# Kernel tuning notes

Hardware: AMD Instinct MI355X
Metric: run time of the kernel (lower is better)

Reference implementation:

```python
import jax, jax.numpy as jnp
import numpy as np

CLUSTER_TEMP = 5.0


def setup_inputs() -> dict:
    key = jax.random.key(0)
    ks = jax.random.split(key, 8)
    n, d_in, h, d, K = 50000, 512, 1024, 256, 64
    s = lambda f: 1.0 / np.sqrt(f)
    return {
        "x": jax.random.normal(ks[0], (n, d_in), dtype=jnp.float32),
        "W1": jax.random.normal(ks[1], (d_in, h), dtype=jnp.float32) * s(d_in),
        "b1": jnp.zeros((h,), jnp.float32),
        "W2": jax.random.normal(ks[2], (h, h), dtype=jnp.float32) * s(h),
        "b2": jnp.zeros((h,), jnp.float32),
        "W3": jax.random.normal(ks[3], (h, d), dtype=jnp.float32) * s(h),
        "b3": jnp.zeros((d,), jnp.float32),
        "mu_init": jax.random.normal(ks[4], (K, d), dtype=jnp.float32),
        "num_iter": 10,
    }


def reference(x, W1, b1, W2, b2, W3, b3, mu_init, num_iter):
    # MLP embed: ReLU on all but last layer
    h1 = jax.nn.relu(x @ W1 + b1)
    h2 = jax.nn.relu(h1 @ W2 + b2)
    embeds = h2 @ W3 + b3                      # [n, d]

    # row-wise L2 normalize (torch.diag(1/norm) @ data == row scaling)
    data = embeds / jnp.linalg.norm(embeds, axis=1, keepdims=True)

    def step(mu, _):
        dist = data @ mu.T                     # [n, K]
        r = jax.nn.softmax(CLUSTER_TEMP * dist, axis=1)
        cluster_r = r.sum(axis=0)              # [K]
        cluster_mean = jnp.einsum('nk,nd->kd', r, data)  # [K, d]
        new_mu = cluster_mean / cluster_r[:, None]       # diag(1/cluster_r) @ mean
        return new_mu, None

    mu, _ = jax.lax.scan(step, mu_init, None, length=num_iter)
    dist = data @ mu.T
    r = jax.nn.softmax(CLUSTER_TEMP * dist, axis=1)      # forward returns r only
    return r
```

## Files before the change

### kernel.cpp

```cpp
#include <hip/hip_runtime.h>
#include <math.h>

#define CLUSTER_TEMP 5.0f
#define NSPL 16

typedef __attribute__((ext_vector_type(8))) short bf16x8;
typedef __attribute__((ext_vector_type(4))) float f32x4;

__device__ __forceinline__ unsigned short f2bf(float f) {
  unsigned u = __float_as_uint(f);
  u += 0x7fff + ((u >> 16) & 1);
  return (unsigned short)(u >> 16);
}
__device__ __forceinline__ float bf2f(unsigned short s) {
  return __uint_as_float((unsigned)s << 16);
}

typedef const __attribute__((address_space(1))) void* gas_t;
typedef __attribute__((address_space(3))) void* las_t;
__device__ __forceinline__ void gload16(const void* g, void* l) {
  __builtin_amdgcn_global_load_lds((gas_t)g, (las_t)l, 16, 0, 0);
}

__global__ __launch_bounds__(256)
void wprep(const float* __restrict__ W, unsigned short* __restrict__ hi,
           unsigned short* __restrict__ lo, int K, int N)
{
  __shared__ float tile[32][33];
  const int bx = blockIdx.x * 32;
  const int by = blockIdx.y * 32;
  const int tx = threadIdx.x, ty = threadIdx.y;
#pragma unroll
  for (int i = 0; i < 4; ++i)
    tile[ty + i*8][tx] = W[(size_t)(by + ty + i*8)*N + bx + tx];
  __syncthreads();
#pragma unroll
  for (int i = 0; i < 4; ++i) {
    const int nn = bx + ty + i*8;
    const int kk = by + tx;
    const float v = tile[tx][ty + i*8];
    const unsigned short h = f2bf(v);
    hi[(size_t)nn*K + kk] = h;
    lo[(size_t)nn*K + kk] = f2bf(v - bf2f(h));
  }
}

template<int INMODE, bool RELU, bool PAIR_OUT>
__global__ __launch_bounds__(256, 2)
void gemm_pair(const float* __restrict__ Af,
               const unsigned short* __restrict__ Ah, const unsigned short* __restrict__ Al,
               const unsigned short* __restrict__ Bh, const unsigned short* __restrict__ Bl,
               const float* __restrict__ bias,
               unsigned short* __restrict__ Ch, unsigned short* __restrict__ Cl,
               float* __restrict__ Cf,
               int M, int N, int K)
{
  __shared__ unsigned short As_h[128][32];
  __shared__ unsigned short As_l[128][32];
  __shared__ unsigned short Bs_h[128][32];
  __shared__ unsigned short Bs_l[128][32];
  const int t = threadIdx.x, l = t & 63, w = t >> 6;
  const int wm = w >> 1, wn = w & 1;
  const int fr = l & 15, fq = l >> 4;

  const int gx = gridDim.x;
  const int total = gx * gridDim.y;
  const int flat = blockIdx.y * gx + blockIdx.x;
  const int q = total >> 3, rmd = total & 7;
  const int xcd = flat & 7, pos = flat >> 3;
  const int nid = (xcd < rmd ? xcd * (q + 1) : rmd * (q + 1) + (xcd - rmd) * q) + pos;
  const int row0 = (nid / gx) * 128;
  const int col0 = (nid % gx) * 128;

  const int srow = l >> 2;
  const int scol = (l & 3) * 8;

  f32x4 acc[4][4];
#pragma unroll
  for (int i = 0; i < 4; ++i)
#pragma unroll
    for (int j = 0; j < 4; ++j) {
      acc[i][j][0]=0.f; acc[i][j][1]=0.f; acc[i][j][2]=0.f; acc[i][j][3]=0.f;
    }

  for (int k0 = 0; k0 < K; k0 += 32) {
    __syncthreads();
    if constexpr (INMODE == 0) {
#pragma unroll
      for (int i = 0; i < 4; ++i) {
        const int f = t + i*256;
        const int r = f >> 3, c4 = (f & 7) * 4;
        const int ra = min(row0 + r, M - 1);
        const float4 v = *(const float4*)(Af + (size_t)ra*K + k0 + c4);
        ushort4 hv, lv;
        hv.x = f2bf(v.x); lv.x = f2bf(v.x - bf2f(hv.x));
        hv.y = f2bf(v.y); lv.y = f2bf(v.y - bf2f(hv.y));
        hv.z = f2bf(v.z); lv.z = f2bf(v.z - bf2f(hv.z));
        hv.w = f2bf(v.w); lv.w = f2bf(v.w - bf2f(hv.w));
        *(ushort4*)&As_h[r][c4] = hv;
        *(ushort4*)&As_l[r][c4] = lv;
      }
#pragma unroll
      for (int j = 0; j < 2; ++j) {
        const int chunk = w*2 + j;
        const int rl = chunk*16 + srow;
        const size_t bo = (size_t)(col0 + rl)*K + k0 + scol;
        gload16(Bh + bo, &Bs_h[chunk*16][0]);
        gload16(Bl + bo, &Bs_l[chunk*16][0]);
      }
    } else {
#pragma unroll
      for (int j = 0; j < 2; ++j) {
        const int chunk = w*2 + j;
        const int rl = chunk*16 + srow;
        const int ra = min(row0 + rl, M-1);
        const size_t ao = (size_t)ra*K + k0 + scol;
        const size_t bo = (size_t)(col0 + rl)*K + k0 + scol;
        gload16(Ah + ao, &As_h[chunk*16][0]);
        gload16(Al + ao, &As_l[chunk*16][0]);
        gload16(Bh + bo, &Bs_h[chunk*16][0]);
        gload16(Bl + bo, &Bs_l[chunk*16][0]);
      }
    }
    __syncthreads();

    bf16x8 ah[4], al[4], bh[4], bl[4];
#pragma unroll
    for (int i = 0; i < 4; ++i) {
      ah[i] = *(const bf16x8*)&As_h[wm*64 + i*16 + fr][fq*8];
      al[i] = *(const bf16x8*)&As_l[wm*64 + i*16 + fr][fq*8];
      bh[i] = *(const bf16x8*)&Bs_h[wn*64 + i*16 + fr][fq*8];
      bl[i] = *(const bf16x8*)&Bs_l[wn*64 + i*16 + fr][fq*8];
    }
#pragma unroll
    for (int i = 0; i < 4; ++i)
#pragma unroll
      for (int j = 0; j < 4; ++j) {
        acc[i][j] = __builtin_amdgcn_mfma_f32_16x16x32_bf16(ah[i], bh[j], acc[i][j], 0, 0, 0);
        acc[i][j] = __builtin_amdgcn_mfma_f32_16x16x32_bf16(ah[i], bl[j], acc[i][j], 0, 0, 0);
        acc[i][j] = __builtin_amdgcn_mfma_f32_16x16x32_bf16(al[i], bh[j], acc[i][j], 0, 0, 0);
      }
  }

  float bj[4];
#pragma unroll
  for (int j = 0; j < 4; ++j) bj[j] = bias[col0 + wn*64 + j*16 + fr];

#pragma unroll
  for (int i = 0; i < 4; ++i)
#pragma unroll
    for (int qq = 0; qq < 4; ++qq) {
      const int r = row0 + wm*64 + i*16 + fq*4 + qq;
      if (r < M) {
#pragma unroll
        for (int j = 0; j < 4; ++j) {
          float v = acc[i][j][qq] + bj[j];
          if constexpr (RELU) v = fmaxf(v, 0.f);
          const int cidx = col0 + wn*64 + j*16 + fr;
          if constexpr (PAIR_OUT) {
            const unsigned short h = f2bf(v);
            Ch[(size_t)r*N + cidx] = h;
            Cl[(size_t)r*N + cidx] = f2bf(v - bf2f(h));
          } else {
            Cf[(size_t)r*N + cidx] = v;
          }
        }
      }
    }
}

__global__ __launch_bounds__(256)
void normsplit(const float* __restrict__ E,
               unsigned short* __restrict__ dsph, unsigned short* __restrict__ dspl,
               unsigned short* __restrict__ dshT,
               int n, int nt)
{
  __shared__ float tile[64][260];
  __shared__ float nrm[4][64];
  __shared__ float invr[64];
  const int t = threadIdx.x;
  const int n0 = blockIdx.x * 64;
#pragma unroll
  for (int i = 0; i < 16; ++i) {
    const int flat = t + i*256;
    const int r = flat >> 6, c4 = (flat & 63) * 4;
    const int rg = min(n0 + r, n - 1);
    *(float4*)&tile[r][c4] = *(const float4*)(E + (size_t)rg*256 + c4);
  }
  __syncthreads();
  {
    const int r = t & 63, qq = t >> 6;
    float s = 0.f;
#pragma unroll
    for (int j = 0; j < 64; ++j) { const float v = tile[r][qq*64 + j]; s = fmaf(v, v, s); }
    nrm[qq][r] = s;
  }
  __syncthreads();
  if (t < 64) invr[t] = 1.0f / sqrtf(nrm[0][t] + nrm[1][t] + nrm[2][t] + nrm[3][t]);
  __syncthreads();
#pragma unroll
  for (int i = 0; i < 16; ++i) {
    const int flat = t + i*256;
    const int r = flat >> 6, c4 = (flat & 63) * 4;
    float4 v = *(const float4*)&tile[r][c4];
    const float iv = invr[r];
    v.x *= iv; v.y *= iv; v.z *= iv; v.w *= iv;
    ushort4 h, lo;
    h.x = f2bf(v.x); lo.x = f2bf(v.x - bf2f(h.x));
    h.y = f2bf(v.y); lo.y = f2bf(v.y - bf2f(h.y));
    h.z = f2bf(v.z); lo.z = f2bf(v.z - bf2f(h.z));
    h.w = f2bf(v.w); lo.w = f2bf(v.w - bf2f(h.w));
    const int rg = n0 + r;
    const int rb = rg >> 4, fr = rg & 15;
    const int ks = c4 >> 5, g = (c4 >> 3) & 3, j = c4 & 7;
    const size_t o = ((size_t)(rb*8 + ks)*64 + g*16 + fr)*8 + j;
    *(ushort4*)(dsph + o) = h;
    *(ushort4*)(dspl + o) = lo;
  }
  const int dd = t >> 3;
  const int nseg = t & 7;
#pragma unroll
  for (int dgrp = 0; dgrp < 8; ++dgrp) {
    const int d = dgrp*32 + dd;
    union { unsigned short s[8]; uint4 u; } hb;
#pragma unroll
    for (int j = 0; j < 8; ++j) {
      const int r = nseg*8 + j;
      hb.s[j] = f2bf(tile[r][d] * invr[r]);
    }
    *(uint4*)(dshT + (size_t)d*nt + n0 + nseg*8) = hb.u;
  }
}

__device__ __forceinline__ size_t mu_off(int k, int d) {
  return ((size_t)((k >> 4)*8 + (d >> 5))*64 + ((d >> 3) & 3)*16 + (k & 15))*8 + (d & 7);
}

__global__ __launch_bounds__(256)
void musplit0(const float* __restrict__ mu0, unsigned short* __restrict__ muPh,
              unsigned short* __restrict__ muPl)
{
  const int i = blockIdx.x*256 + threadIdx.x;
  const int k = i >> 8, d = i & 255;
  const float v = mu0[i];
  const unsigned short h = f2bf(v);
  const size_t o = mu_off(k, d);
  muPh[o] = h; muPl[o] = f2bf(v - bf2f(h));
}

template<bool FINAL>
__global__ __launch_bounds__(512, 4)
void cluster_iter(const unsigned short* __restrict__ dsph, const unsigned short* __restrict__ dspl,
                  const unsigned short* __restrict__ dshT,
                  const unsigned short* __restrict__ muPh, const unsigned short* __restrict__ muPl,
                  float* __restrict__ acc_g,
                  float* __restrict__ out, int n, int nt)
{
  __shared__ unsigned short pt_h[64][136];
  __shared__ float crp[8][64];
  const int t = threadIdx.x, l = t & 63, w = t >> 6;
  const int fr = l & 15, g = l >> 4;
  const int base = blockIdx.x * 128;
  const int rb = (base >> 4) + w;

  f32x4 dacc[4];
#pragma unroll
  for (int nf = 0; nf < 4; ++nf) {
    dacc[nf][0]=0.f; dacc[nf][1]=0.f; dacc[nf][2]=0.f; dacc[nf][3]=0.f;
  }
#pragma unroll
  for (int ks = 0; ks < 8; ++ks) {
    const size_t ao = ((size_t)(rb*8 + ks)*64 + l)*8;
    const bf16x8 Ah = *(const bf16x8*)(dsph + ao);
    const bf16x8 Al = *(const bf16x8*)(dspl + ao);
#pragma unroll
    for (int nf = 0; nf < 4; ++nf) {
      const size_t bo = ((size_t)(nf*8 + ks)*64 + l)*8;
      const bf16x8 Bh = *(const bf16x8*)(muPh + bo);
      const bf16x8 Bl = *(const bf16x8*)(muPl + bo);
      dacc[nf] = __builtin_amdgcn_mfma_f32_16x16x32_bf16(Ah, Bh, dacc[nf], 0, 0, 0);
      dacc[nf] = __builtin_amdgcn_mfma_f32_16x16x32_bf16(Ah, Bl, dacc[nf], 0, 0, 0);
      dacc[nf] = __builtin_amdgcn_mfma_f32_16x16x32_bf16(Al, Bh, dacc[nf], 0, 0, 0);
    }
  }

  float accr[4] = {0.f, 0.f, 0.f, 0.f};
  {
    float mx[4], se[4], p[4][4];
#pragma unroll
    for (int r = 0; r < 4; ++r) {
      mx[r] = fmaxf(fmaxf(dacc[0][r], dacc[1][r]), fmaxf(dacc[2][r], dacc[3][r]));
#pragma unroll
      for (int off = 1; off < 16; off <<= 1) mx[r] = fmaxf(mx[r], __shfl_xor(mx[r], off));
      se[r] = 0.f;
    }
#pragma unroll
    for (int nf = 0; nf < 4; ++nf)
#pragma unroll
      for (int r = 0; r < 4; ++r) {
        p[nf][r] = __expf(CLUSTER_TEMP * (dacc[nf][r] - mx[r]));
        se[r] += p[nf][r];
      }
#pragma unroll
    for (int r = 0; r < 4; ++r) {
#pragma unroll
      for (int off = 1; off < 16; off <<= 1) se[r] += __shfl_xor(se[r], off);
      se[r] = 1.0f / se[r];
    }
    if (FINAL) {
#pragma unroll
      for (int r = 0; r < 4; ++r) {
        const int rowg = base + 16*w + 4*g + r;
        if (rowg < n) {
#pragma unroll
          for (int nf = 0; nf < 4; ++nf)
            out[(size_t)rowg*64 + nf*16 + fr] = p[nf][r] * se[r];
        }
      }
    } else {
      float sc[4];
#pragma unroll
      for (int r = 0; r < 4; ++r) {
        const int rowg = base + 16*w + 4*g + r;
        sc[r] = (rowg < n) ? se[r] : 0.f;
      }
      const int rowb = 16*w + 4*g;
#pragma unroll
      for (int nf = 0; nf < 4; ++nf) {
        ushort4 hv;
        float s4 = 0.f;
#pragma unroll
        for (int r = 0; r < 4; ++r) {
          const float P = p[nf][r] * sc[r];
          s4 += P;
          ((unsigned short*)&hv)[r] = f2bf(P);
        }
        accr[nf] += s4;
        *(ushort4*)&pt_h[nf*16 + fr][rowb] = hv;
      }
    }
  }

  if (FINAL) return;

#pragma unroll
  for (int nf = 0; nf < 4; ++nf) {
    accr[nf] += __shfl_xor(accr[nf], 16);
    accr[nf] += __shfl_xor(accr[nf], 32);
  }
  if (l < 16) {
#pragma unroll
    for (int nf = 0; nf < 4; ++nf) crp[w][nf*16 + l] = accr[nf];
  }
  __syncthreads();

  f32x4 acc2[4][2];
#pragma unroll
  for (int i = 0; i < 4; ++i)
#pragma unroll
    for (int j = 0; j < 2; ++j) {
      acc2[i][j][0]=0.f; acc2[i][j][1]=0.f; acc2[i][j][2]=0.f; acc2[i][j][3]=0.f;
    }
#pragma unroll
  for (int ks = 0; ks < 4; ++ks) {
    bf16x8 Ph[4];
#pragma unroll
    for (int mf = 0; mf < 4; ++mf)
      Ph[mf] = *(const bf16x8*)&pt_h[mf*16 + fr][ks*32 + 8*g];
#pragma unroll
    for (int nf = 0; nf < 2; ++nf) {
      const size_t bo = (size_t)(32*w + nf*16 + fr)*nt + base + ks*32 + 8*g;
      const bf16x8 Bh = *(const bf16x8*)(dshT + bo);
#pragma unroll
      for (int mf = 0; mf < 4; ++mf)
        acc2[mf][nf] = __builtin_amdgcn_mfma_f32_16x16x32_bf16(Ph[mf], Bh, acc2[mf][nf], 0, 0, 0);
    }
  }

  float* accs = acc_g + (size_t)(blockIdx.x & (NSPL-1)) * 16448;
#pragma unroll
  for (int mf = 0; mf < 4; ++mf)
#pragma unroll
    for (int nf = 0; nf < 2; ++nf)
#pragma unroll
      for (int r = 0; r < 4; ++r)
        atomicAdd(&accs[(size_t)(mf*16 + 4*g + r)*256 + 32*w + nf*16 + fr],
                  acc2[mf][nf][r]);
  if (t < 64)
    atomicAdd(&accs[16384 + t],
              crp[0][t] + crp[1][t] + crp[2][t] + crp[3][t] +
              crp[4][t] + crp[5][t] + crp[6][t] + crp[7][t]);
}

__global__ __launch_bounds__(256)
void musplit_it(float* __restrict__ acc_g,
                unsigned short* __restrict__ muPh, unsigned short* __restrict__ muPl)
{
  const int k = blockIdx.x;
  const int d = threadIdx.x;
  float v = 0.f, r = 0.f;
#pragma unroll
  for (int c = 0; c < NSPL; ++c) {
    v += acc_g[(size_t)c*16448 + (size_t)k*256 + d];
    r += acc_g[(size_t)c*16448 + 16384 + k];
  }
  v /= r;
  __syncthreads();
  const size_t o = mu_off(k, d);
  const unsigned short h = f2bf(v);
  muPh[o] = h; muPl[o] = f2bf(v - bf2f(h));
#pragma unroll
  for (int c = 0; c < NSPL; ++c)
    acc_g[(size_t)c*16448 + (size_t)k*256 + d] = 0.f;
  if (d < NSPL) acc_g[(size_t)d*16448 + 16384 + k] = 0.f;
}

extern "C" void kernel_launch(void* const* d_in, const int* in_sizes, int n_in,
                              void* d_out, int out_size, void* d_ws, size_t ws_size,
                              hipStream_t stream)
{
  const float* x   = (const float*)d_in[0];
  const float* W1  = (const float*)d_in[1];
  const float* b1  = (const float*)d_in[2];
  const float* W2  = (const float*)d_in[3];
  const float* b2  = (const float*)d_in[4];
  const float* W3  = (const float*)d_in[5];
  const float* b3  = (const float*)d_in[6];
  const float* mu0 = (const float*)d_in[7];
  const int DIN = 512, H = 1024, D = 256, ITERS = 10;
  const int n = in_sizes[0] / DIN;
  const int NP = ((n + 127) / 128) * 128;
  const int NT = (n + 64 + 255) & ~255;
  const int NBK = NP / 128;

  char* ws = (char*)d_ws;
  const size_t MB = 1024*1024;
  const size_t nH2 = (size_t)n * H * 2;
  unsigned short* h1h = (unsigned short*)ws;
  unsigned short* h1l = (unsigned short*)(ws + nH2);
  unsigned short* h2h = (unsigned short*)(ws + 2*nH2);
  unsigned short* h2l = (unsigned short*)(ws + 3*nH2);
  float* data = (float*)ws;
  unsigned short* dsph = (unsigned short*)(ws + 52*MB);
  unsigned short* dspl = (unsigned short*)(ws + 78*MB);
  unsigned short* dshT = (unsigned short*)(ws + 104*MB);
  float* acc_g  = (float*)(ws + 180*MB);
  unsigned short* muPh = (unsigned short*)(ws + 183*MB);
  unsigned short* muPl = (unsigned short*)(ws + 184*MB);

  unsigned short* w1th = (unsigned short*)d_out;
  unsigned short* w1tl = w1th + (size_t)H*DIN;
  unsigned short* w2th = w1tl + (size_t)H*DIN;
  unsigned short* w2tl = w2th + (size_t)H*H;
  unsigned short* w3th = w2tl + (size_t)H*H;
  unsigned short* w3tl = w3th + (size_t)D*H;

  hipMemsetAsync(acc_g, 0, (size_t)NSPL * 16448 * sizeof(float), stream);

  wprep<<<dim3(H/32, DIN/32), dim3(32,8), 0, stream>>>(W1, w1th, w1tl, DIN, H);
  wprep<<<dim3(H/32, H/32),   dim3(32,8), 0, stream>>>(W2, w2th, w2tl, H, H);
  wprep<<<dim3(D/32, H/32),   dim3(32,8), 0, stream>>>(W3, w3th, w3tl, H, D);

  const int gy = (n + 127) / 128;
  gemm_pair<0, true,  true ><<<dim3(H/128, gy), 256, 0, stream>>>(
      x, nullptr, nullptr, w1th, w1tl, b1, h1h, h1l, nullptr, n, H, DIN);
  gemm_pair<1, true,  true ><<<dim3(H/128, gy), 256, 0, stream>>>(
      nullptr, h1h, h1l, w2th, w2tl, b2, h2h, h2l, nullptr, n, H, H);
  gemm_pair<1, false, false><<<dim3(D/128, gy), 256, 0, stream>>>(
      nullptr, h2h, h2l, w3th, w3tl, b3, nullptr, nullptr, data, n, D, H);

  normsplit<<<dim3(NT/64), dim3(256), 0, stream>>>(data, dsph, dspl, dshT, n, NT);
  musplit0<<<dim3(64), dim3(256), 0, stream>>>(mu0, muPh, muPl);

  for (int it = 0; it < ITERS; ++it) {
    cluster_iter<false><<<dim3(NBK), dim3(512), 0, stream>>>(
        dsph, dspl, dshT, muPh, muPl, acc_g, nullptr, n, NT);
    musplit_it<<<dim3(64), dim3(256), 0, stream>>>(acc_g, muPh, muPl);
  }
  cluster_iter<true><<<dim3(NBK), dim3(512), 0, stream>>>(
      dsph, dspl, dshT, muPh, muPl, nullptr, (float*)d_out, n, NT);
}
```

Before: 1.054 ms.

## Add 256x256-tile 8-wave split-bf16 GEMM for layers two and three

Adds a new GEMM kernel with 256x256 output tiles, 512 threads (8 waves), double-buffered LDS staging through direct global-to-LDS loads, an XCD-aware block remap, swizzled LDS offsets and raised MFMA priority. The second and third MLP layers now use it in place of the 128x128 kernel. Larger tiles raise arithmetic intensity and cut redundant operand loads. In exchange they lower occupancy to one block per CU and leave fewer blocks in the grid, especially for the 256-wide last layer, which gets only one column of tiles.

```diff
diff --git a/kernel.cpp b/kernel.cpp
--- a/kernel.cpp
+++ b/kernel.cpp
@@ -151,6 +151,126 @@
 #pragma unroll
     for (int qq = 0; qq < 4; ++qq) {
       const int r = row0 + wm*64 + i*16 + fq*4 + qq;
+      if (r < M) {
+#pragma unroll
+        for (int j = 0; j < 4; ++j) {
+          float v = acc[i][j][qq] + bj[j];
+          if constexpr (RELU) v = fmaxf(v, 0.f);
+          const int cidx = col0 + wn*64 + j*16 + fr;
+          if constexpr (PAIR_OUT) {
+            const unsigned short h = f2bf(v);
+            Ch[(size_t)r*N + cidx] = h;
+            Cl[(size_t)r*N + cidx] = f2bf(v - bf2f(h));
+          } else {
+            Cf[(size_t)r*N + cidx] = v;
+          }
+        }
+      }
+    }
+}
+
+template<bool RELU, bool PAIR_OUT>
+__global__ __launch_bounds__(512, 1)
+void gemm8p(const unsigned short* __restrict__ Ah, const unsigned short* __restrict__ Al,
+            const unsigned short* __restrict__ Bh, const unsigned short* __restrict__ Bl,
+            const float* __restrict__ bias,
+            unsigned short* __restrict__ Ch, unsigned short* __restrict__ Cl,
+            float* __restrict__ Cf,
+            int M, int N, int K)
+{
+  __shared__ unsigned short lds[2][4][8192];
+  const int t = threadIdx.x, l = t & 63, w = t >> 6;
+  const int wm = w >> 2, wn = w & 3;
+  const int fr = l & 15, fq = l >> 4;
+  const int fq_eff = ((fq + (fr >> 1)) & 3) * 8;
+
+  const int gx = gridDim.x;
+  const int total = gx * gridDim.y;
+  const int flat = blockIdx.y * gx + blockIdx.x;
+  const int q = total >> 3, rmd = total & 7;
+  const int xcd = flat & 7, pos = flat >> 3;
+  const int nid = (xcd < rmd ? xcd * (q + 1) : rmd * (q + 1) + (xcd - rmd) * q) + pos;
+  const int row0 = (nid / gx) * 256;
+  const int col0 = (nid % gx) * 256;
+
+  const int st_row = w*16 + (l >> 2);
+  const int st_fqs = (((l & 3) - (l >> 3)) & 3) * 8;
+
+  auto STG_A = [&](int kt, int d, int h) {
+    const int kk = kt*32 + st_fqs;
+    const int ar = min(row0 + h*128 + st_row, M - 1);
+    const int lb = h*4096 + w*512;
+    gload16(Ah + (size_t)ar*K + kk, &lds[d][0][lb]);
+    gload16(Al + (size_t)ar*K + kk, &lds[d][1][lb]);
+  };
+  auto STG_B = [&](int kt, int d, int h) {
+    const int kk = kt*32 + st_fqs;
+    const int br = col0 + h*128 + st_row;
+    const int lb = h*4096 + w*512;
+    gload16(Bh + (size_t)br*K + kk, &lds[d][2][lb]);
+    gload16(Bl + (size_t)br*K + kk, &lds[d][3][lb]);
+  };
+
+  f32x4 acc[8][4];
+#pragma unroll
+  for (int i = 0; i < 8; ++i)
+#pragma unroll
+    for (int j = 0; j < 4; ++j) {
+      acc[i][j][0]=0.f; acc[i][j][1]=0.f; acc[i][j][2]=0.f; acc[i][j][3]=0.f;
+    }
+
+  const int NKT = K >> 5;
+  STG_A(0, 0, 0); STG_A(0, 0, 1); STG_B(0, 0, 0); STG_B(0, 0, 1);
+
+  for (int kt = 0; kt < NKT; ++kt) {
+    const int d = kt & 1;
+    const bool pre = (kt + 1 < NKT);
+    asm volatile("s_waitcnt vmcnt(0)" ::: "memory");
+    __builtin_amdgcn_s_barrier();
+
+    bf16x8 Bhf[4], Blf[4];
+#pragma unroll
+    for (int j = 0; j < 4; ++j) {
+      const int off = (wn*64 + j*16 + fr)*32 + fq_eff;
+      Bhf[j] = *(const bf16x8*)&lds[d][2][off];
+      Blf[j] = *(const bf16x8*)&lds[d][3][off];
+    }
+#pragma unroll
+    for (int p = 0; p < 4; ++p) {
+      if (p == 0 && pre) { STG_A(kt+1, d^1, 0); STG_A(kt+1, d^1, 1); }
+      if (p == 1 && pre) { STG_B(kt+1, d^1, 0); STG_B(kt+1, d^1, 1); }
+      bf16x8 Ahf[2], Alf[2];
+#pragma unroll
+      for (int ii = 0; ii < 2; ++ii) {
+        const int off = (wm*128 + (p*2 + ii)*16 + fr)*32 + fq_eff;
+        Ahf[ii] = *(const bf16x8*)&lds[d][0][off];
+        Alf[ii] = *(const bf16x8*)&lds[d][1][off];
+      }
+      __builtin_amdgcn_s_setprio(1);
+#pragma unroll
+      for (int ii = 0; ii < 2; ++ii) {
+        const int mi = p*2 + ii;
+#pragma unroll
+        for (int j = 0; j < 4; ++j) {
+          acc[mi][j] = __builtin_amdgcn_mfma_f32_16x16x32_bf16(Ahf[ii], Bhf[j], acc[mi][j], 0, 0, 0);
+          acc[mi][j] = __builtin_amdgcn_mfma_f32_16x16x32_bf16(Ahf[ii], Blf[j], acc[mi][j], 0, 0, 0);
+          acc[mi][j] = __builtin_amdgcn_mfma_f32_16x16x32_bf16(Alf[ii], Bhf[j], acc[mi][j], 0, 0, 0);
+        }
+      }
+      __builtin_amdgcn_s_setprio(0);
+      __builtin_amdgcn_s_barrier();
+    }
+  }
+
+  float bj[4];
+#pragma unroll
+  for (int j = 0; j < 4; ++j) bj[j] = bias[col0 + wn*64 + j*16 + fr];
+
+#pragma unroll
+  for (int i = 0; i < 8; ++i)
+#pragma unroll
+    for (int qq = 0; qq < 4; ++qq) {
+      const int r = row0 + wm*128 + i*16 + fq*4 + qq;
       if (r < M) {
 #pragma unroll
         for (int j = 0; j < 4; ++j) {
@@ -461,13 +581,14 @@
   wprep<<<dim3(H/32, H/32),   dim3(32,8), 0, stream>>>(W2, w2th, w2tl, H, H);
   wprep<<<dim3(D/32, H/32),   dim3(32,8), 0, stream>>>(W3, w3th, w3tl, H, D);
 
-  const int gy = (n + 127) / 128;
-  gemm_pair<0, true,  true ><<<dim3(H/128, gy), 256, 0, stream>>>(
+  const int gy128 = (n + 127) / 128;
+  const int gy256 = (n + 255) / 256;
+  gemm_pair<0, true, true><<<dim3(H/128, gy128), 256, 0, stream>>>(
       x, nullptr, nullptr, w1th, w1tl, b1, h1h, h1l, nullptr, n, H, DIN);
-  gemm_pair<1, true,  true ><<<dim3(H/128, gy), 256, 0, stream>>>(
-      nullptr, h1h, h1l, w2th, w2tl, b2, h2h, h2l, nullptr, n, H, H);
-  gemm_pair<1, false, false><<<dim3(D/128, gy), 256, 0, stream>>>(
-      nullptr, h2h, h2l, w3th, w3tl, b3, nullptr, nullptr, data, n, D, H);
+  gemm8p<true,  true ><<<dim3(H/256, gy256), 512, 0, stream>>>(
+      h1h, h1l, w2th, w2tl, b2, h2h, h2l, nullptr, n, H, H);
+  gemm8p<false, false><<<dim3(D/256, gy256), 512, 0, stream>>>(
+      h2h, h2l, w3th, w3tl, b3, nullptr, nullptr, data, n, D, H);
 
   normsplit<<<dim3(NT/64), dim3(256), 0, stream>>>(data, dsph, dspl, dshT, n, NT);
   musplit0<<<dim3(64), dim3(256), 0, stream>>>(mu0, muPh, muPl);
```

New measurement: 1.040 ms. No clear change (-1.3%).
